# Optimization experiments

Measured on AMD Instinct MI355X. Metric: run time of the kernel, lower is better.

The kernel has to match this reference:

```python
import jax, jax.numpy as jnp
import numpy as np

NUM_HEADS = 8

def setup_inputs() -> dict:
    key0 = jax.random.key(0)
    ks = jax.random.split(key0, 12)
    L, S, N, E, Dh = 1024, 1024, 8, 512, 64
    w_scale = 1.0 / np.sqrt(E)
    return {
        "query": jax.random.normal(ks[0], (L, N, E), jnp.float32),
        "key": jax.random.normal(ks[1], (S, N, E), jnp.float32),
        "value": jax.random.normal(ks[2], (S, N, E), jnp.float32),
        "pos_k": jax.random.normal(ks[3], (L, S, Dh), jnp.float32) * 0.1,
        "pos_v": jax.random.normal(ks[4], (L, S, Dh), jnp.float32) * 0.1,
        "Wq": jax.random.normal(ks[5], (E, E), jnp.float32) * w_scale,
        "bq": jnp.zeros((E,), jnp.float32),
        "Wk": jax.random.normal(ks[6], (E, E), jnp.float32) * w_scale,
        "bk": jnp.zeros((E,), jnp.float32),
        "Wv": jax.random.normal(ks[7], (E, E), jnp.float32) * w_scale,
        "bv": jnp.zeros((E,), jnp.float32),
        "Wo": jax.random.normal(ks[8], (E, E), jnp.float32) * w_scale,
        "bo": jnp.zeros((E,), jnp.float32),
    }


def reference(query, key, value, pos_k, pos_v, Wq, bq, Wk, bk, Wv, bv, Wo, bo):
    L, N, E = query.shape
    S = key.shape[0]
    H = NUM_HEADS
    Dh = E // H
    scaling = Dh ** -0.5

    # separate Q/K/V projections (torch Linear: x @ W.T + b)
    q = (query @ Wq.T + bq) * scaling          # (L, N, E)
    k = key @ Wk.T + bk                        # (S, N, E)
    v = value @ Wv.T + bv                      # (S, N, E)

    # (L, N*H, Dh) -> (N*H, L, Dh), matching torch's view+transpose
    q = q.reshape(L, N * H, Dh).transpose(1, 0, 2)
    k = k.reshape(S, N * H, Dh).transpose(1, 0, 2)
    v = v.reshape(S, N * H, Dh).transpose(1, 0, 2)

    # content scores + relative-position key term B
    scores = jnp.einsum('bld,bsd->bls', q, k)          # (N*H, L, S)
    scores = scores + jnp.einsum('bld,lsd->bls', q, pos_k)

    # mine_softmax: clamp to finfo.min (turns -inf into finite min), then softmax
    scores = jnp.maximum(scores, jnp.finfo(scores.dtype).min)
    w = jax.nn.softmax(scores, axis=-1)                # (N*H, L, S)

    # attention output + relative-position value term
    out = jnp.einsum('bls,bsd->bld', w, v) + jnp.einsum('bls,lsd->bld', w, pos_v)
    out = out.transpose(1, 0, 2).reshape(L, N, E)
    attn_output = out @ Wo.T + bo                      # (L, N, E)

    # averaged attention weights over heads: (N, L, S)
    avg_w = w.reshape(N, H, L, S).sum(axis=1) / H
    return attn_output, avg_w
```

## Files before the change

### kernel.cpp

```cpp
#include <hip/hip_runtime.h>
#include <hip/hip_bf16.h>
#include <hip/hip_fp16.h>


typedef float     f32x4  __attribute__((ext_vector_type(4)));
typedef _Float16  f16x8  __attribute__((ext_vector_type(8)));
typedef _Float16  f16x4  __attribute__((ext_vector_type(4)));

#define MFMA_F16  __builtin_amdgcn_mfma_f32_16x16x32_f16

__device__ __forceinline__ f16x8 ld8f(const float* __restrict__ p){
  const f32x4 a = *(const f32x4*)p;
  const f32x4 b = *(const f32x4*)(p + 4);
  f16x8 h;
#pragma unroll
  for (int t = 0; t < 4; ++t) { h[t] = (_Float16)a[t]; h[t + 4] = (_Float16)b[t]; }
  return h;
}

__device__ __forceinline__ f16x8 cvt8(f32x4 a, f32x4 b){
  f16x8 h;
#pragma unroll
  for (int t = 0; t < 4; ++t) { h[t] = (_Float16)a[t]; h[t + 4] = (_Float16)b[t]; }
  return h;
}

__global__ __launch_bounds__(256) void proj_all(
    const float* __restrict__ Xq, const float* __restrict__ Xk, const float* __restrict__ Xv,
    const float* __restrict__ Wq, const float* __restrict__ Wk, const float* __restrict__ Wv,
    const float* __restrict__ bq, const float* __restrict__ bk, const float* __restrict__ bv,
    _Float16* __restrict__ qb, _Float16* __restrict__ kb, _Float16* __restrict__ vT)
{
  __shared__ _Float16 As[128][40];
  __shared__ _Float16 Bs[128][40];

  const int which = blockIdx.z;
  const float* X    = (which == 0) ? Xq : (which == 1) ? Xk : Xv;
  const float* W    = (which == 0) ? Wq : (which == 1) ? Wk : Wv;
  const float* bias = (which == 0) ? bq : (which == 1) ? bk : bv;
  _Float16*   out   = (which == 0) ? qb : (which == 1) ? kb : vT;
  const float scale = (which == 0) ? 0.125f : 1.0f;
  const int   mode  = (which == 2) ? 1 : 0;

  const int tid = threadIdx.x, wave = tid >> 6, lane = tid & 63;
  const int lrow = lane & 15, quad = lane >> 4;
  const int wr = wave >> 1, wc = wave & 1;
  const int m_base = blockIdx.x * 128;
  const int n_base = blockIdx.y * 128;
  const int srow = tid >> 2, scol = (tid & 3) * 8;

  const float* xp0 = X + (size_t)(m_base + srow)      * 512 + scol;
  const float* xp1 = X + (size_t)(m_base + 64 + srow) * 512 + scol;
  const float* wp0 = W + (size_t)(n_base + srow)      * 512 + scol;
  const float* wp1 = W + (size_t)(n_base + 64 + srow) * 512 + scol;

  f32x4 ra0, ra1, rb0, rb1, rc0, rc1, rd0, rd1;
  auto LOADK = [&](int k0) {
    ra0 = *(const f32x4*)(xp0 + k0);  ra1 = *(const f32x4*)(xp0 + k0 + 4);
    rb0 = *(const f32x4*)(xp1 + k0);  rb1 = *(const f32x4*)(xp1 + k0 + 4);
    rc0 = *(const f32x4*)(wp0 + k0);  rc1 = *(const f32x4*)(wp0 + k0 + 4);
    rd0 = *(const f32x4*)(wp1 + k0);  rd1 = *(const f32x4*)(wp1 + k0 + 4);
  };

  f32x4 acc[4][4] = {};
  LOADK(0);
  for (int k0 = 0; k0 < 512; k0 += 32) {
    __syncthreads();
    *(f16x8*)&As[srow][scol]      = cvt8(ra0, ra1);
    *(f16x8*)&As[srow + 64][scol] = cvt8(rb0, rb1);
    *(f16x8*)&Bs[srow][scol]      = cvt8(rc0, rc1);
    *(f16x8*)&Bs[srow + 64][scol] = cvt8(rd0, rd1);
    __syncthreads();
    if (k0 + 32 < 512) LOADK(k0 + 32);
    f16x8 af[4], bf[4];
#pragma unroll
    for (int mi = 0; mi < 4; ++mi)
      af[mi] = *(const f16x8*)&As[wr * 64 + mi * 16 + lrow][quad * 8];
#pragma unroll
    for (int ni = 0; ni < 4; ++ni)
      bf[ni] = *(const f16x8*)&Bs[wc * 64 + ni * 16 + lrow][quad * 8];
#pragma unroll
    for (int mi = 0; mi < 4; ++mi)
#pragma unroll
      for (int ni = 0; ni < 4; ++ni)
        acc[mi][ni] = MFMA_F16(af[mi], bf[ni], acc[mi][ni], 0, 0, 0);
  }

#pragma unroll
  for (int mi = 0; mi < 4; ++mi)
#pragma unroll
  for (int ni = 0; ni < 4; ++ni) {
    const int ncol = n_base + wc * 64 + ni * 16 + lrow;
    const float bv2 = bias[ncol];
#pragma unroll
    for (int r = 0; r < 4; ++r) {
      const int m = m_base + wr * 64 + mi * 16 + quad * 4 + r;
      const float val = (acc[mi][ni][r] + bv2) * scale;
      if (mode == 0) {
        out[(size_t)m * 512 + ncol] = (_Float16)val;
      } else {
        const int s = m >> 3, nn = m & 7, h = ncol >> 6, d = ncol & 63;
        out[(size_t)(nn * 8 + h) * 65536 + (size_t)d * 1024 + s] = (_Float16)val;
      }
    }
  }
}

__global__ __launch_bounds__(256) void out_gemm(
    const _Float16* __restrict__ X, const float* __restrict__ W,
    const float* __restrict__ bias, float* __restrict__ out)
{
  __shared__ _Float16 As[128][40];
  __shared__ _Float16 Bs[128][40];

  const int tid = threadIdx.x, wave = tid >> 6, lane = tid & 63;
  const int lrow = lane & 15, quad = lane >> 4;
  const int wr = wave >> 1, wc = wave & 1;
  const int m_base = blockIdx.x * 128;
  const int n_base = blockIdx.y * 128;
  const int srow = tid >> 2, scol = (tid & 3) * 8;

  const _Float16* xp0 = X + (size_t)(m_base + srow)      * 512 + scol;
  const _Float16* xp1 = X + (size_t)(m_base + 64 + srow) * 512 + scol;
  const float*    wp0 = W + (size_t)(n_base + srow)      * 512 + scol;
  const float*    wp1 = W + (size_t)(n_base + 64 + srow) * 512 + scol;

  f16x8 ha, hb; f32x4 rc0, rc1, rd0, rd1;
  auto LOADK = [&](int k0) {
    ha  = *(const f16x8*)(xp0 + k0);
    hb  = *(const f16x8*)(xp1 + k0);
    rc0 = *(const f32x4*)(wp0 + k0);  rc1 = *(const f32x4*)(wp0 + k0 + 4);
    rd0 = *(const f32x4*)(wp1 + k0);  rd1 = *(const f32x4*)(wp1 + k0 + 4);
  };

  f32x4 acc[4][4] = {};
  LOADK(0);
  for (int k0 = 0; k0 < 512; k0 += 32) {
    __syncthreads();
    *(f16x8*)&As[srow][scol]      = ha;
    *(f16x8*)&As[srow + 64][scol] = hb;
    *(f16x8*)&Bs[srow][scol]      = cvt8(rc0, rc1);
    *(f16x8*)&Bs[srow + 64][scol] = cvt8(rd0, rd1);
    __syncthreads();
    if (k0 + 32 < 512) LOADK(k0 + 32);
    f16x8 af[4], bf[4];
#pragma unroll
    for (int mi = 0; mi < 4; ++mi)
      af[mi] = *(const f16x8*)&As[wr * 64 + mi * 16 + lrow][quad * 8];
#pragma unroll
    for (int ni = 0; ni < 4; ++ni)
      bf[ni] = *(const f16x8*)&Bs[wc * 64 + ni * 16 + lrow][quad * 8];
#pragma unroll
    for (int mi = 0; mi < 4; ++mi)
#pragma unroll
      for (int ni = 0; ni < 4; ++ni)
        acc[mi][ni] = MFMA_F16(af[mi], bf[ni], acc[mi][ni], 0, 0, 0);
  }

#pragma unroll
  for (int mi = 0; mi < 4; ++mi)
#pragma unroll
  for (int ni = 0; ni < 4; ++ni) {
    const int ncol = n_base + wc * 64 + ni * 16 + lrow;
    const float bv2 = bias[ncol];
#pragma unroll
    for (int r = 0; r < 4; ++r) {
      const int m = m_base + wr * 64 + mi * 16 + quad * 4 + r;
      out[(size_t)m * 512 + ncol] = acc[mi][ni][r] + bv2;
    }
  }
}

__global__ __launch_bounds__(256) void qk_content(
    const _Float16* __restrict__ qb, const _Float16* __restrict__ kb,
    _Float16* __restrict__ sbuf)
{
  const int b = blockIdx.z;
  const int tid = threadIdx.x, wave = tid >> 6, lane = tid & 63;
  const int lrow = lane & 15, quad = lane >> 4;
  const int l_base = blockIdx.x * 64 + (wave >> 1) * 32;
  const int s_base = blockIdx.y * 64 + (wave & 1) * 32;
  const _Float16* qp = qb + b * 64;
  const _Float16* kp = kb + b * 64;
  f32x4 acc[2][2] = {};
#pragma unroll
  for (int k0 = 0; k0 < 64; k0 += 32) {
    const int ko = k0 + quad * 8;
    f16x8 a0 = *(const f16x8*)(qp + (size_t)(l_base + lrow) * 4096 + ko);
    f16x8 a1 = *(const f16x8*)(qp + (size_t)(l_base + 16 + lrow) * 4096 + ko);
    f16x8 b0 = *(const f16x8*)(kp + (size_t)(s_base + lrow) * 4096 + ko);
    f16x8 b1 = *(const f16x8*)(kp + (size_t)(s_base + 16 + lrow) * 4096 + ko);
    acc[0][0] = MFMA_F16(a0, b0, acc[0][0], 0, 0, 0);
    acc[0][1] = MFMA_F16(a0, b1, acc[0][1], 0, 0, 0);
    acc[1][0] = MFMA_F16(a1, b0, acc[1][0], 0, 0, 0);
    acc[1][1] = MFMA_F16(a1, b1, acc[1][1], 0, 0, 0);
  }
#pragma unroll
  for (int i = 0; i < 2; ++i)
#pragma unroll
  for (int j = 0; j < 2; ++j)
#pragma unroll
  for (int r = 0; r < 4; ++r) {
    const size_t idx = (size_t)(l_base + i * 16 + quad * 4 + r) * 65536 +
                       (size_t)b * 1024 + s_base + j * 16 + lrow;
    sbuf[idx] = (_Float16)acc[i][j][r];
  }
}

__global__ __launch_bounds__(512, 4) void pos_softmax_avg(
    const _Float16* __restrict__ qb, const float* __restrict__ pk,
    _Float16* __restrict__ sbuf, float* __restrict__ avg_out)
{
  __shared__ float pmax[2][4][16];
  __shared__ float psum[2][4][16];

  const int l = blockIdx.x;
  const int bh = blockIdx.y;
  const int tid = threadIdx.x, wave = tid >> 6, lane = tid & 63;
  const int lrow = lane & 15, quad = lane >> 4;
  const int wb = wave >> 2;
  const int ws = wave & 3;
  const int b0 = bh * 32 + wb * 16;

  const _Float16* qp = qb + (size_t)l * 4096 + (size_t)b0 * 64;
  const float*    pp = pk + (size_t)l * 65536 + (size_t)(ws * 256) * 64;
  _Float16*       sp = sbuf + (size_t)l * 65536;

  f16x8 bq[2];
#pragma unroll
  for (int ks = 0; ks < 2; ++ks)
    bq[ks] = *(const f16x8*)(qp + (size_t)lrow * 64 + ks * 32 + quad * 8);

  f32x4 acc[16] = {};
#pragma unroll
  for (int t = 0; t < 16; ++t) {
#pragma unroll
    for (int ks = 0; ks < 2; ++ks) {
      const f16x8 a = ld8f(pp + (size_t)(t * 16 + lrow) * 64 + ks * 32 + quad * 8);
      acc[t] = MFMA_F16(a, bq[ks], acc[t], 0, 0, 0);
    }
  }

  const _Float16* crow = sp + (size_t)(b0 + lrow) * 1024 + ws * 256 + quad * 4;
#pragma unroll
  for (int t = 0; t < 16; ++t) {
    const f16x4 c = *(const f16x4*)(crow + t * 16);
#pragma unroll
    for (int r = 0; r < 4; ++r) acc[t][r] += (float)c[r];
  }

  float mw = acc[0][0];
#pragma unroll
  for (int t = 0; t < 16; ++t)
#pragma unroll
    for (int r = 0; r < 4; ++r) mw = fmaxf(mw, acc[t][r]);
  mw = fmaxf(mw, __shfl_xor(mw, 16));
  mw = fmaxf(mw, __shfl_xor(mw, 32));

  float zw = 0.f;
#pragma unroll
  for (int t = 0; t < 16; ++t)
#pragma unroll
    for (int r = 0; r < 4; ++r) { acc[t][r] = __expf(acc[t][r] - mw); zw += acc[t][r]; }
  zw += __shfl_xor(zw, 16);
  zw += __shfl_xor(zw, 32);

  if (lane < 16) { pmax[wb][ws][lrow] = mw; psum[wb][ws][lrow] = zw; }
  __syncthreads();

  float M = pmax[wb][0][lrow];
#pragma unroll
  for (int o = 1; o < 4; ++o) M = fmaxf(M, pmax[wb][o][lrow]);
  float Z = 0.f;
#pragma unroll
  for (int o = 0; o < 4; ++o) Z += psum[wb][o][lrow] * __expf(pmax[wb][o][lrow] - M);
  const float scl = __expf(mw - M) / Z;

  _Float16* wrow = sp + (size_t)(b0 + lrow) * 1024 + ws * 256 + quad * 4;
  const int n = (b0 + lrow) >> 3;
  float* ao = avg_out + (size_t)n * 1048576 + (size_t)l * 1024 + ws * 256 + quad * 4;
  const bool wr_avg = ((lane & 7) == 0);
#pragma unroll
  for (int t = 0; t < 16; ++t) {
    f16x4 wv; f32x4 av;
#pragma unroll
    for (int r = 0; r < 4; ++r) {
      const float w = acc[t][r] * scl;
      wv[r] = (_Float16)w;
      float hsum = w;
      hsum += __shfl_xor(hsum, 1);
      hsum += __shfl_xor(hsum, 2);
      hsum += __shfl_xor(hsum, 4);
      av[r] = hsum * 0.125f;
    }
    *(f16x4*)(wrow + t * 16) = wv;
    if (wr_avg) *(f32x4*)(ao + t * 16) = av;
  }
}

__global__ __launch_bounds__(256) void pv_content(
    const _Float16* __restrict__ sbuf, const _Float16* __restrict__ vT,
    float* __restrict__ ctx)
{
  const int b = blockIdx.x;
  const int tid = threadIdx.x, wave = tid >> 6, lane = tid & 63;
  const int lrow = lane & 15, quad = lane >> 4;
  const int l_base = blockIdx.y * 64 + (wave >> 1) * 32;
  const int d_base = (wave & 1) * 32;
  const _Float16* wp = sbuf + (size_t)b * 1024;
  const _Float16* vp = vT + (size_t)b * 65536;
  f32x4 acc[2][2] = {};
  for (int s0 = 0; s0 < 1024; s0 += 32) {
    const int so = s0 + quad * 8;
    f16x8 a0 = *(const f16x8*)(wp + (size_t)(l_base + lrow) * 65536 + so);
    f16x8 a1 = *(const f16x8*)(wp + (size_t)(l_base + 16 + lrow) * 65536 + so);
    f16x8 b0 = *(const f16x8*)(vp + (size_t)(d_base + lrow) * 1024 + so);
    f16x8 b1 = *(const f16x8*)(vp + (size_t)(d_base + 16 + lrow) * 1024 + so);
    acc[0][0] = MFMA_F16(a0, b0, acc[0][0], 0, 0, 0);
    acc[0][1] = MFMA_F16(a0, b1, acc[0][1], 0, 0, 0);
    acc[1][0] = MFMA_F16(a1, b0, acc[1][0], 0, 0, 0);
    acc[1][1] = MFMA_F16(a1, b1, acc[1][1], 0, 0, 0);
  }
#pragma unroll
  for (int i = 0; i < 2; ++i)
#pragma unroll
  for (int j = 0; j < 2; ++j)
#pragma unroll
  for (int r = 0; r < 4; ++r)
    ctx[(size_t)(l_base + i * 16 + quad * 4 + r) * 4096 + b * 64 + d_base + j * 16 + lrow] =
        acc[i][j][r];
}

__global__ __launch_bounds__(256) void pv_pos(
    const _Float16* __restrict__ sbuf, const float* __restrict__ pv,
    const float* __restrict__ ctx, _Float16* __restrict__ ctx2)
{
  __shared__ _Float16 lds[64][72];
  const int l = blockIdx.x;
  const int tid = threadIdx.x, wave = tid >> 6, lane = tid & 63;
  const int lrow = lane & 15, quad = lane >> 4;
  const int b_base = (wave >> 1) * 32;
  const int d_base = (wave & 1) * 32;
  const float* pp = pv + (size_t)l * 65536;
  const _Float16* wp = sbuf + (size_t)l * 65536;
  const int st_s = tid >> 2, st_d = (tid & 3) * 16;
  f32x4 acc[2][2] = {};
  for (int s0 = 0; s0 < 1024; s0 += 64) {
    __syncthreads();
    const float* src = pp + (size_t)(s0 + st_s) * 64 + st_d;
    const f32x4 va = *(const f32x4*)src;
    const f32x4 vb = *(const f32x4*)(src + 4);
    const f32x4 vc = *(const f32x4*)(src + 8);
    const f32x4 vd = *(const f32x4*)(src + 12);
#pragma unroll
    for (int u = 0; u < 4; ++u) {
      lds[st_d + u     ][st_s] = (_Float16)va[u];
      lds[st_d + u + 4 ][st_s] = (_Float16)vb[u];
      lds[st_d + u + 8 ][st_s] = (_Float16)vc[u];
      lds[st_d + u + 12][st_s] = (_Float16)vd[u];
    }
    __syncthreads();
#pragma unroll
    for (int k0 = 0; k0 < 64; k0 += 32) {
      const int so = s0 + k0 + quad * 8;
      const int sl = k0 + quad * 8;
      f16x8 a0 = *(const f16x8*)(wp + (size_t)(b_base + lrow) * 1024 + so);
      f16x8 a1 = *(const f16x8*)(wp + (size_t)(b_base + 16 + lrow) * 1024 + so);
      f16x8 b0 = *(const f16x8*)(&lds[d_base + lrow][sl]);
      f16x8 b1 = *(const f16x8*)(&lds[d_base + 16 + lrow][sl]);
      acc[0][0] = MFMA_F16(a0, b0, acc[0][0], 0, 0, 0);
      acc[0][1] = MFMA_F16(a0, b1, acc[0][1], 0, 0, 0);
      acc[1][0] = MFMA_F16(a1, b0, acc[1][0], 0, 0, 0);
      acc[1][1] = MFMA_F16(a1, b1, acc[1][1], 0, 0, 0);
    }
  }
#pragma unroll
  for (int i = 0; i < 2; ++i)
#pragma unroll
  for (int j = 0; j < 2; ++j)
#pragma unroll
  for (int r = 0; r < 4; ++r) {
    const size_t idx = (size_t)l * 4096 + (size_t)(b_base + i * 16 + quad * 4 + r) * 64 +
                       d_base + j * 16 + lrow;
    ctx2[idx] = (_Float16)(ctx[idx] + acc[i][j][r]);
  }
}

extern "C" void kernel_launch(void* const* d_in, const int* in_sizes, int n_in,
                              void* d_out, int out_size, void* d_ws, size_t ws_size,
                              hipStream_t stream)
{
  const float* query = (const float*)d_in[0];
  const float* key   = (const float*)d_in[1];
  const float* value = (const float*)d_in[2];
  const float* pos_k = (const float*)d_in[3];
  const float* pos_v = (const float*)d_in[4];
  const float* Wq = (const float*)d_in[5];
  const float* bq = (const float*)d_in[6];
  const float* Wk = (const float*)d_in[7];
  const float* bk = (const float*)d_in[8];
  const float* Wv = (const float*)d_in[9];
  const float* bv = (const float*)d_in[10];
  const float* Wo = (const float*)d_in[11];
  const float* bo = (const float*)d_in[12];

  char* ws = (char*)d_ws;
  _Float16* qb   = (_Float16*)(ws);
  _Float16* kb   = (_Float16*)(ws + (size_t)(8u  << 20));
  _Float16* vT   = (_Float16*)(ws + (size_t)(16u << 20));
  _Float16* sbuf = (_Float16*)(ws + (size_t)(24u << 20));
  float*    ctx  = (float*)   (ws + (size_t)(152u << 20));
  _Float16* ctx2 = (_Float16*)(ws + (size_t)(168u << 20));

  float* out0 = (float*)d_out;
  float* avg  = out0 + (size_t)4194304;

  dim3 blk(256);
  proj_all<<<dim3(64, 4, 3), blk, 0, stream>>>(query, key, value,
                                               Wq, Wk, Wv, bq, bk, bv,
                                               qb, kb, vT);
  qk_content<<<dim3(16, 16, 64), blk, 0, stream>>>(qb, kb, sbuf);
  pos_softmax_avg<<<dim3(1024, 2), dim3(512), 0, stream>>>(qb, pos_k, sbuf, avg);
  pv_content<<<dim3(64, 16), blk, 0, stream>>>(sbuf, vT, ctx);
  pv_pos<<<dim3(1024), blk, 0, stream>>>(sbuf, pos_v, ctx, ctx2);
  out_gemm<<<dim3(64, 4), blk, 0, stream>>>(ctx2, Wo, bo, out0);
}
```

Measured before the change: 954.3 us.

## Process all heads per query row in pos-softmax to reuse pos_k loads

The positional-score softmax kernel now launches one block per query row covering all 64 batch-heads instead of splitting heads across two blocks. Each wave handles 128 key positions and applies every loaded pos_k fragment to four head groups, so pos_k is read from memory once rather than twice. The cross-wave softmax reduction is widened to 8 partial maxima/sums per head. This doubles the per-thread accumulator count, increasing register pressure and possibly reducing occupancy.

```diff
diff --git a/kernel.cpp b/kernel.cpp
--- a/kernel.cpp
+++ b/kernel.cpp
@@ -195,6 +195,7 @@
     acc[1][0] = MFMA_F16(a1, b0, acc[1][0], 0, 0, 0);
     acc[1][1] = MFMA_F16(a1, b1, acc[1][1], 0, 0, 0);
   }
+  _Float16* sp = sbuf + (size_t)b * 1024;
 #pragma unroll
   for (int i = 0; i < 2; ++i)
 #pragma unroll
@@ -202,99 +203,121 @@
 #pragma unroll
   for (int r = 0; r < 4; ++r) {
     const size_t idx = (size_t)(l_base + i * 16 + quad * 4 + r) * 65536 +
-                       (size_t)b * 1024 + s_base + j * 16 + lrow;
-    sbuf[idx] = (_Float16)acc[i][j][r];
-  }
-}
-
-__global__ __launch_bounds__(512, 4) void pos_softmax_avg(
+                       s_base + j * 16 + lrow;
+    sp[idx] = (_Float16)acc[i][j][r];
+  }
+}
+
+__global__ __launch_bounds__(512) void pos_softmax_avg(
     const _Float16* __restrict__ qb, const float* __restrict__ pk,
     _Float16* __restrict__ sbuf, float* __restrict__ avg_out)
 {
-  __shared__ float pmax[2][4][16];
-  __shared__ float psum[2][4][16];
+  __shared__ float pmax[8][64];
+  __shared__ float psum[8][64];
 
   const int l = blockIdx.x;
-  const int bh = blockIdx.y;
-  const int tid = threadIdx.x, wave = tid >> 6, lane = tid & 63;
-  const int lrow = lane & 15, quad = lane >> 4;
-  const int wb = wave >> 2;
-  const int ws = wave & 3;
-  const int b0 = bh * 32 + wb * 16;
-
-  const _Float16* qp = qb + (size_t)l * 4096 + (size_t)b0 * 64;
-  const float*    pp = pk + (size_t)l * 65536 + (size_t)(ws * 256) * 64;
+  const int tid = threadIdx.x, wave = tid >> 6, lane = tid & 63;
+  const int lrow = lane & 15, quad = lane >> 4;
+  const int s_base = wave * 128;
+
+  const _Float16* qp = qb + (size_t)l * 4096;
+  const float*    pp = pk + (size_t)l * 65536 + (size_t)s_base * 64;
   _Float16*       sp = sbuf + (size_t)l * 65536;
 
-  f16x8 bq[2];
-#pragma unroll
-  for (int ks = 0; ks < 2; ++ks)
-    bq[ks] = *(const f16x8*)(qp + (size_t)lrow * 64 + ks * 32 + quad * 8);
-
-  f32x4 acc[16] = {};
-#pragma unroll
-  for (int t = 0; t < 16; ++t) {
+  f16x8 bq[4][2];
+#pragma unroll
+  for (int bc = 0; bc < 4; ++bc)
+#pragma unroll
+    for (int ks = 0; ks < 2; ++ks)
+      bq[bc][ks] = *(const f16x8*)(qp + (size_t)(bc * 16 + lrow) * 64 + ks * 32 + quad * 8);
+
+  f32x4 acc[8][4];
+#pragma unroll
+  for (int t = 0; t < 8; ++t)
+#pragma unroll
+    for (int bc = 0; bc < 4; ++bc) {
+      const f16x4 c = *(const f16x4*)(sp + (size_t)(bc * 16 + lrow) * 1024 +
+                                      s_base + t * 16 + quad * 4);
+#pragma unroll
+      for (int r = 0; r < 4; ++r) acc[t][bc][r] = (float)c[r];
+    }
+
+#pragma unroll
+  for (int t = 0; t < 8; ++t) {
 #pragma unroll
     for (int ks = 0; ks < 2; ++ks) {
       const f16x8 a = ld8f(pp + (size_t)(t * 16 + lrow) * 64 + ks * 32 + quad * 8);
-      acc[t] = MFMA_F16(a, bq[ks], acc[t], 0, 0, 0);
-    }
-  }
-
-  const _Float16* crow = sp + (size_t)(b0 + lrow) * 1024 + ws * 256 + quad * 4;
-#pragma unroll
-  for (int t = 0; t < 16; ++t) {
-    const f16x4 c = *(const f16x4*)(crow + t * 16);
-#pragma unroll
-    for (int r = 0; r < 4; ++r) acc[t][r] += (float)c[r];
-  }
-
-  float mw = acc[0][0];
-#pragma unroll
-  for (int t = 0; t < 16; ++t)
-#pragma unroll
-    for (int r = 0; r < 4; ++r) mw = fmaxf(mw, acc[t][r]);
-  mw = fmaxf(mw, __shfl_xor(mw, 16));
-  mw = fmaxf(mw, __shfl_xor(mw, 32));
-
-  float zw = 0.f;
-#pragma unroll
-  for (int t = 0; t < 16; ++t)
-#pragma unroll
-    for (int r = 0; r < 4; ++r) { acc[t][r] = __expf(acc[t][r] - mw); zw += acc[t][r]; }
-  zw += __shfl_xor(zw, 16);
-  zw += __shfl_xor(zw, 32);
-
-  if (lane < 16) { pmax[wb][ws][lrow] = mw; psum[wb][ws][lrow] = zw; }
+#pragma unroll
+      for (int bc = 0; bc < 4; ++bc)
+        acc[t][bc] = MFMA_F16(a, bq[bc][ks], acc[t][bc], 0, 0, 0);
+    }
+  }
+
+  float mw[4], zw[4];
+#pragma unroll
+  for (int bc = 0; bc < 4; ++bc) {
+    float m = acc[0][bc][0];
+#pragma unroll
+    for (int t = 0; t < 8; ++t)
+#pragma unroll
+      for (int r = 0; r < 4; ++r) m = fmaxf(m, acc[t][bc][r]);
+    m = fmaxf(m, __shfl_xor(m, 16));
+    m = fmaxf(m, __shfl_xor(m, 32));
+    float z = 0.f;
+#pragma unroll
+    for (int t = 0; t < 8; ++t)
+#pragma unroll
+      for (int r = 0; r < 4; ++r) { acc[t][bc][r] = __expf(acc[t][bc][r] - m); z += acc[t][bc][r]; }
+    z += __shfl_xor(z, 16);
+    z += __shfl_xor(z, 32);
+    mw[bc] = m; zw[bc] = z;
+  }
+
+  if (lane < 16) {
+#pragma unroll
+    for (int bc = 0; bc < 4; ++bc) {
+      pmax[wave][bc * 16 + lrow] = mw[bc];
+      psum[wave][bc * 16 + lrow] = zw[bc];
+    }
+  }
   __syncthreads();
 
-  float M = pmax[wb][0][lrow];
-#pragma unroll
-  for (int o = 1; o < 4; ++o) M = fmaxf(M, pmax[wb][o][lrow]);
-  float Z = 0.f;
-#pragma unroll
-  for (int o = 0; o < 4; ++o) Z += psum[wb][o][lrow] * __expf(pmax[wb][o][lrow] - M);
-  const float scl = __expf(mw - M) / Z;
-
-  _Float16* wrow = sp + (size_t)(b0 + lrow) * 1024 + ws * 256 + quad * 4;
-  const int n = (b0 + lrow) >> 3;
-  float* ao = avg_out + (size_t)n * 1048576 + (size_t)l * 1024 + ws * 256 + quad * 4;
+  float scl[4];
+#pragma unroll
+  for (int bc = 0; bc < 4; ++bc) {
+    const int b = bc * 16 + lrow;
+    float M = pmax[0][b];
+#pragma unroll
+    for (int o = 1; o < 8; ++o) M = fmaxf(M, pmax[o][b]);
+    float Z = 0.f;
+#pragma unroll
+    for (int o = 0; o < 8; ++o) Z += psum[o][b] * __expf(pmax[o][b] - M);
+    scl[bc] = __expf(mw[bc] - M) / Z;
+  }
+
   const bool wr_avg = ((lane & 7) == 0);
 #pragma unroll
-  for (int t = 0; t < 16; ++t) {
-    f16x4 wv; f32x4 av;
-#pragma unroll
-    for (int r = 0; r < 4; ++r) {
-      const float w = acc[t][r] * scl;
-      wv[r] = (_Float16)w;
-      float hsum = w;
-      hsum += __shfl_xor(hsum, 1);
-      hsum += __shfl_xor(hsum, 2);
-      hsum += __shfl_xor(hsum, 4);
-      av[r] = hsum * 0.125f;
-    }
-    *(f16x4*)(wrow + t * 16) = wv;
-    if (wr_avg) *(f32x4*)(ao + t * 16) = av;
+  for (int t = 0; t < 8; ++t) {
+#pragma unroll
+    for (int bc = 0; bc < 4; ++bc) {
+      f16x4 wv; f32x4 av;
+#pragma unroll
+      for (int r = 0; r < 4; ++r) {
+        const float w = acc[t][bc][r] * scl[bc];
+        wv[r] = (_Float16)w;
+        float hsum = w;
+        hsum += __shfl_xor(hsum, 1);
+        hsum += __shfl_xor(hsum, 2);
+        hsum += __shfl_xor(hsum, 4);
+        av[r] = hsum * 0.125f;
+      }
+      *(f16x4*)(sp + (size_t)(bc * 16 + lrow) * 1024 + s_base + t * 16 + quad * 4) = wv;
+      if (wr_avg) {
+        const int n = (bc * 16 + lrow) >> 3;
+        *(f32x4*)(avg_out + (size_t)n * 1048576 + (size_t)l * 1024 +
+                  s_base + t * 16 + quad * 4) = av;
+      }
+    }
   }
 }
 
@@ -420,7 +443,7 @@
                                                Wq, Wk, Wv, bq, bk, bv,
                                                qb, kb, vT);
   qk_content<<<dim3(16, 16, 64), blk, 0, stream>>>(qb, kb, sbuf);
-  pos_softmax_avg<<<dim3(1024, 2), dim3(512), 0, stream>>>(qb, pos_k, sbuf, avg);
+  pos_softmax_avg<<<dim3(1024), dim3(512), 0, stream>>>(qb, pos_k, sbuf, avg);
   pv_content<<<dim3(64, 16), blk, 0, stream>>>(sbuf, vT, ctx);
   pv_pos<<<dim3(1024), blk, 0, stream>>>(sbuf, pos_v, ctx, ctx2);
   out_gemm<<<dim3(64, 4), blk, 0, stream>>>(ctx2, Wo, bo, out0);
```

Measured after the change: 871.5 us. 8.7% less time.
